# Performance work log

Measured on AMD Instinct MI355X. Metric: run time of the kernel, lower is better.

The kernel has to match this reference:

```python
import jax, jax.numpy as jnp
import numpy as np
from jax import lax

_SOBEL_X = jnp.array([[-1., 0., 1.], [-2., 0., 2.], [-1., 0., 1.]], dtype=jnp.float32)
_SOBEL_Y = jnp.array([[1., 2., 1.], [0., 0., 0.], [-1., -2., -1.]], dtype=jnp.float32)


def rgb2ycrcb(x):
    # x: [B,3,H,W] -> [B,3,H,W] (Y, Cr, Cb)
    R, G, B = x[:, 0], x[:, 1], x[:, 2]
    Y = 0.299 * R + 0.587 * G + 0.114 * B
    Cr = (R - Y) * 0.713 + 0.5
    Cb = (B - Y) * 0.564 + 0.5
    return jnp.stack([Y, Cr, Cb], axis=1)


def depthwise_sobel(x):
    # x: [B,3,H,W]; per-channel 3x3 cross-correlation with SAME padding (matches F.conv2d pad=1)
    C = x.shape[1]
    wx = jnp.broadcast_to(_SOBEL_X[None, None], (C, 1, 3, 3))
    wy = jnp.broadcast_to(_SOBEL_Y[None, None], (C, 1, 3, 3))
    dn = ('NCHW', 'OIHW', 'NCHW')
    gx = lax.conv_general_dilated(x, wx, (1, 1), 'SAME', feature_group_count=C, dimension_numbers=dn)
    gy = lax.conv_general_dilated(x, wy, (1, 1), 'SAME', feature_group_count=C, dimension_numbers=dn)
    return gx, gy


def adjust_gamma(img, gamma, gain=1.0):
    # torchvision float path: clamp(gain * img**gamma, 0, 1)
    return jnp.clip(gain * img ** gamma, 0.0, 1.0)


def adjust_contrast(img, factor):
    # torchvision: blend with per-image mean of grayscale, then clamp
    gray = 0.2989 * img[:, 0:1] + 0.587 * img[:, 1:2] + 0.114 * img[:, 2:3]
    mean = jnp.mean(gray, axis=(1, 2, 3), keepdims=True)
    return jnp.clip(factor * img + (1.0 - factor) * mean, 0.0, 1.0)


def l1(a, b):
    return jnp.mean(jnp.abs(a - b))


def fusion_loss(input_vis, input_ir, output, Mask):
    Fuse = output * Mask
    ycc_fuse = rgb2ycrcb(Fuse)
    Cr_F, Cb_F = ycc_fuse[:, 1:2], ycc_fuse[:, 2:3]

    R_vis = adjust_gamma(input_vis, 0.5, 1.0)
    ycc_vis = rgb2ycrcb(R_vis)
    Cr_V, Cb_V = ycc_vis[:, 1:2], ycc_vis[:, 2:3]

    R_ir = adjust_contrast(input_ir, 1.8)

    fgx, fgy = depthwise_sobel(Fuse)
    vgx, vgy = depthwise_sobel(R_vis)
    igx, igy = depthwise_sobel(R_ir)

    joint_gx = jnp.maximum(vgx, igx)
    joint_gy = jnp.maximum(vgy, igy)
    joint_int = jnp.maximum(R_vis, R_ir)

    con_loss = l1(Fuse, joint_int)
    grad_loss = 0.5 * l1(fgx, joint_gx) + 0.5 * l1(fgy, joint_gy)
    color_loss = l1(Cb_F, Cb_V) + l1(Cr_F, Cr_V)
    return 0.5 * con_loss + 0.2 * grad_loss + 1.0 * color_loss


def setup_inputs() -> dict:
    key = jax.random.key(0)
    k1, k2, k3, k4 = jax.random.split(key, 4)
    B, C, H, W = 16, 3, 512, 512
    return {
        'input_vis': jax.random.uniform(k1, (B, C, H, W), dtype=jnp.float32),
        'input_ir': jax.random.uniform(k2, (B, C, H, W), dtype=jnp.float32),
        'output': jax.random.uniform(k3, (B, C, H, W), dtype=jnp.float32),
        'Mask': jax.random.uniform(k4, (B, C, H, W), dtype=jnp.float32),
    }


def reference(input_vis, input_ir, output, Mask):
    return fusion_loss(input_vis, input_ir, output, Mask)
```

## Files before the change

kernel.cpp:

```cpp
#include <hip/hip_runtime.h>
#include <math.h>

#define Bn 16
#define Cn 3
#define Hn 512
#define Wn 512
#define HWn (Hn*Wn)
#define CHWn (Cn*HWn)
#define Rr 8

__device__ __forceinline__ float clamp01(float x) {
    return fminf(fmaxf(x, 0.0f), 1.0f);
}

__global__ __launch_bounds__(256) void gray_mean_kernel(
        const float* __restrict__ ir, float* __restrict__ ws)
{
    const int b = blockIdx.y;
    const int tid = threadIdx.x;
    const float* base = ir + (size_t)b * CHWn;

    float sr = 0.f, sg = 0.f, sb = 0.f;
#pragma unroll
    for (int k = 0; k < 8; ++k) {
        size_t px = (size_t)blockIdx.x * 8192 + (size_t)(k * 256 + tid) * 4;
        float4 r4 = *(const float4*)(base + px);
        float4 g4 = *(const float4*)(base + HWn + px);
        float4 b4 = *(const float4*)(base + 2 * HWn + px);
        sr += (r4.x + r4.y) + (r4.z + r4.w);
        sg += (g4.x + g4.y) + (g4.z + g4.w);
        sb += (b4.x + b4.y) + (b4.z + b4.w);
    }
    float s = 0.2989f * sr + 0.587f * sg + 0.114f * sb;

#pragma unroll
    for (int off = 32; off; off >>= 1) s += __shfl_down(s, off, 64);

    __shared__ float red[4];
    if ((tid & 63) == 0) red[tid >> 6] = s;
    __syncthreads();
    if (tid == 0) atomicAdd(&ws[b], (red[0] + red[1]) + (red[2] + red[3]));
}

__global__ __launch_bounds__(256) void fusion_main_kernel(
        const float* __restrict__ vis, const float* __restrict__ ir,
        const float* __restrict__ outp, const float* __restrict__ mask,
        float* __restrict__ ws)
{
    const int tid = threadIdx.x;
    const int tx = tid & 127;
    const int sy = tid >> 7;
    const int b  = blockIdx.y;
    const int y0 = (blockIdx.x * 2 + sy) * Rr;
    const int x0 = tx * 4;

    const float mean_b = ws[b] * (1.0f / (float)HWn);
    const float moff = 0.8f * mean_b;

    const size_t bb = (size_t)b * CHWn;
    const float* pv = vis  + bb;
    const float* pi = ir   + bb;
    const float* po = outp + bb;
    const float* pm = mask + bb;

    float conA = 0.f, gxA = 0.f, gyA = 0.f;

    for (int c = 0; c < 3; ++c) {
        const float* v_ = pv + (size_t)c * HWn;
        const float* i_ = pi + (size_t)c * HWn;
        const float* o_ = po + (size_t)c * HWn;
        const float* m_ = pm + (size_t)c * HWn;

        float wf[3][6], wv[3][6], wi[3][6];

        auto load_row = [&](int y, int s) {
            if ((unsigned)y < (unsigned)Hn) {
                size_t o = (size_t)y * Wn + x0;
                float4 o4 = *(const float4*)(o_ + o);
                float4 m4 = *(const float4*)(m_ + o);
                float4 v4 = *(const float4*)(v_ + o);
                float4 i4 = *(const float4*)(i_ + o);
                float oL = 0.f, mL = 0.f, vL = 0.f, iL = 0.f;
                float oR = 0.f, mR = 0.f, vR = 0.f, iR = 0.f;
                if (x0 > 0)      { oL = o_[o - 1]; mL = m_[o - 1]; vL = v_[o - 1]; iL = i_[o - 1]; }
                if (x0 + 4 < Wn) { oR = o_[o + 4]; mR = m_[o + 4]; vR = v_[o + 4]; iR = i_[o + 4]; }

                wf[s][0] = oL * mL;     wf[s][1] = o4.x * m4.x;
                wf[s][2] = o4.y * m4.y; wf[s][3] = o4.z * m4.z;
                wf[s][4] = o4.w * m4.w; wf[s][5] = oR * mR;

                wv[s][0] = clamp01(sqrtf(vL));   wv[s][1] = clamp01(sqrtf(v4.x));
                wv[s][2] = clamp01(sqrtf(v4.y)); wv[s][3] = clamp01(sqrtf(v4.z));
                wv[s][4] = clamp01(sqrtf(v4.w)); wv[s][5] = clamp01(sqrtf(vR));

                wi[s][0] = clamp01(fmaf(1.8f, iL,   -moff));
                wi[s][1] = clamp01(fmaf(1.8f, i4.x, -moff));
                wi[s][2] = clamp01(fmaf(1.8f, i4.y, -moff));
                wi[s][3] = clamp01(fmaf(1.8f, i4.z, -moff));
                wi[s][4] = clamp01(fmaf(1.8f, i4.w, -moff));
                wi[s][5] = clamp01(fmaf(1.8f, iR,   -moff));
                if (x0 == 0)       { wf[s][0] = 0.f; wv[s][0] = 0.f; wi[s][0] = 0.f; }
                if (x0 + 4 >= Wn)  { wf[s][5] = 0.f; wv[s][5] = 0.f; wi[s][5] = 0.f; }
            } else {
#pragma unroll
                for (int k = 0; k < 6; ++k) { wf[s][k] = 0.f; wv[s][k] = 0.f; wi[s][k] = 0.f; }
            }
        };

        load_row(y0 - 1, 0);
        load_row(y0,     1);

        for (int yy = 0; yy < Rr; ++yy) {
            load_row(y0 + yy + 1, 2);

#pragma unroll
            for (int j = 0; j < 4; ++j) {
                float gxf = (wf[0][j+2] - wf[0][j]) + 2.f * (wf[1][j+2] - wf[1][j]) + (wf[2][j+2] - wf[2][j]);
                float gyf = (wf[0][j] + 2.f * wf[0][j+1] + wf[0][j+2]) - (wf[2][j] + 2.f * wf[2][j+1] + wf[2][j+2]);

                float gxv = (wv[0][j+2] - wv[0][j]) + 2.f * (wv[1][j+2] - wv[1][j]) + (wv[2][j+2] - wv[2][j]);
                float gyv = (wv[0][j] + 2.f * wv[0][j+1] + wv[0][j+2]) - (wv[2][j] + 2.f * wv[2][j+1] + wv[2][j+2]);

                float gxi = (wi[0][j+2] - wi[0][j]) + 2.f * (wi[1][j+2] - wi[1][j]) + (wi[2][j+2] - wi[2][j]);
                float gyi = (wi[0][j] + 2.f * wi[0][j+1] + wi[0][j+2]) - (wi[2][j] + 2.f * wi[2][j+1] + wi[2][j+2]);

                gxA  += fabsf(gxf - fmaxf(gxv, gxi));
                gyA  += fabsf(gyf - fmaxf(gyv, gyi));
                conA += fabsf(wf[1][j+1] - fmaxf(wv[1][j+1], wi[1][j+1]));
            }

#pragma unroll
            for (int k = 0; k < 6; ++k) {
                wf[0][k] = wf[1][k]; wf[1][k] = wf[2][k];
                wv[0][k] = wv[1][k]; wv[1][k] = wv[2][k];
                wi[0][k] = wi[1][k]; wi[1][k] = wi[2][k];
            }
        }
    }

    float crA = 0.f, cbA = 0.f;
    {
        auto px = [&](float fr, float fg, float fb, float vr, float vg, float vb) {
            float fY = 0.299f * fr + 0.587f * fg + 0.114f * fb;
            float vY = 0.299f * vr + 0.587f * vg + 0.114f * vb;
            float crf = (fr - fY) * 0.713f, crv = (vr - vY) * 0.713f;
            float cbf = (fb - fY) * 0.564f, cbv = (vb - vY) * 0.564f;
            crA += fabsf(crf - crv);
            cbA += fabsf(cbf - cbv);
        };
        for (int y = y0; y < y0 + Rr; ++y) {
            size_t o = (size_t)y * Wn + x0;
            float4 oR = *(const float4*)(po + o);
            float4 oG = *(const float4*)(po + HWn + o);
            float4 oB = *(const float4*)(po + 2 * HWn + o);
            float4 mR = *(const float4*)(pm + o);
            float4 mG = *(const float4*)(pm + HWn + o);
            float4 mB = *(const float4*)(pm + 2 * HWn + o);
            float4 vR = *(const float4*)(pv + o);
            float4 vG = *(const float4*)(pv + HWn + o);
            float4 vB = *(const float4*)(pv + 2 * HWn + o);
            px(oR.x * mR.x, oG.x * mG.x, oB.x * mB.x,
               clamp01(sqrtf(vR.x)), clamp01(sqrtf(vG.x)), clamp01(sqrtf(vB.x)));
            px(oR.y * mR.y, oG.y * mG.y, oB.y * mB.y,
               clamp01(sqrtf(vR.y)), clamp01(sqrtf(vG.y)), clamp01(sqrtf(vB.y)));
            px(oR.z * mR.z, oG.z * mG.z, oB.z * mB.z,
               clamp01(sqrtf(vR.z)), clamp01(sqrtf(vG.z)), clamp01(sqrtf(vB.z)));
            px(oR.w * mR.w, oG.w * mG.w, oB.w * mB.w,
               clamp01(sqrtf(vR.w)), clamp01(sqrtf(vG.w)), clamp01(sqrtf(vB.w)));
        }
    }

    auto wred = [](float x) {
#pragma unroll
        for (int off = 32; off; off >>= 1) x += __shfl_down(x, off, 64);
        return x;
    };
    conA = wred(conA); gxA = wred(gxA); gyA = wred(gyA);
    crA  = wred(crA);  cbA = wred(cbA);

    __shared__ float red[5][4];
    const int lane = tid & 63, w = tid >> 6;
    if (lane == 0) {
        red[0][w] = conA; red[1][w] = gxA; red[2][w] = gyA;
        red[3][w] = crA;  red[4][w] = cbA;
    }
    __syncthreads();
    if (tid < 5) {
        float s = (red[tid][0] + red[tid][1]) + (red[tid][2] + red[tid][3]);
        atomicAdd(&ws[16 + tid], s);
    }
}

__global__ void finalize_kernel(const float* __restrict__ ws, float* __restrict__ out)
{
    if (threadIdx.x == 0 && blockIdx.x == 0) {
        const float invN3 = 1.0f / (float)((size_t)Bn * Cn * HWn);
        const float invN1 = 1.0f / (float)((size_t)Bn * HWn);
        float con = ws[16] * invN3;
        float gx  = ws[17] * invN3;
        float gy  = ws[18] * invN3;
        float cr  = ws[19] * invN1;
        float cb  = ws[20] * invN1;
        out[0] = 0.5f * con + 0.2f * (0.5f * gx + 0.5f * gy) + (cb + cr);
    }
}

extern "C" void kernel_launch(void* const* d_in, const int* in_sizes, int n_in,
                              void* d_out, int out_size, void* d_ws, size_t ws_size,
                              hipStream_t stream)
{
    const float* vis = (const float*)d_in[0];
    const float* ir  = (const float*)d_in[1];
    const float* out = (const float*)d_in[2];
    const float* msk = (const float*)d_in[3];
    float* ws = (float*)d_ws;

    hipMemsetAsync(ws, 0, 32 * sizeof(float), stream);

    gray_mean_kernel<<<dim3(32, Bn), 256, 0, stream>>>(ir, ws);
    fusion_main_kernel<<<dim3(Hn / (2 * Rr), Bn), 256, 0, stream>>>(vis, ir, out, msk, ws);
    finalize_kernel<<<1, 64, 0, stream>>>(ws, (float*)d_out);
}
```

Baseline: 241.4 us.

## Fuse channels and color loss into single rolling-window pass

```diff
diff --git a/kernel.cpp b/kernel.cpp
--- a/kernel.cpp
+++ b/kernel.cpp
@@ -42,17 +42,15 @@
     if (tid == 0) atomicAdd(&ws[b], (red[0] + red[1]) + (red[2] + red[3]));
 }
 
-__global__ __launch_bounds__(256) void fusion_main_kernel(
+__global__ __launch_bounds__(128, 2) void fusion_main_kernel(
         const float* __restrict__ vis, const float* __restrict__ ir,
         const float* __restrict__ outp, const float* __restrict__ mask,
         float* __restrict__ ws)
 {
     const int tid = threadIdx.x;
-    const int tx = tid & 127;
-    const int sy = tid >> 7;
-    const int b  = blockIdx.y;
-    const int y0 = (blockIdx.x * 2 + sy) * Rr;
-    const int x0 = tx * 4;
+    const int b   = blockIdx.y;
+    const int y0  = blockIdx.x * Rr;
+    const int x0  = tid * 4;
 
     const float mean_b = ws[b] * (1.0f / (float)HWn);
     const float moff = 0.8f * mean_b;
@@ -63,110 +61,90 @@
     const float* po = outp + bb;
     const float* pm = mask + bb;
 
-    float conA = 0.f, gxA = 0.f, gyA = 0.f;
-
-    for (int c = 0; c < 3; ++c) {
-        const float* v_ = pv + (size_t)c * HWn;
-        const float* i_ = pi + (size_t)c * HWn;
-        const float* o_ = po + (size_t)c * HWn;
-        const float* m_ = pm + (size_t)c * HWn;
-
-        float wf[3][6], wv[3][6], wi[3][6];
-
-        auto load_row = [&](int y, int s) {
-            if ((unsigned)y < (unsigned)Hn) {
-                size_t o = (size_t)y * Wn + x0;
-                float4 o4 = *(const float4*)(o_ + o);
-                float4 m4 = *(const float4*)(m_ + o);
-                float4 v4 = *(const float4*)(v_ + o);
-                float4 i4 = *(const float4*)(i_ + o);
+    float wf[3][3][6], wv[3][3][6], wi[3][3][6];
+
+    float conA = 0.f, gxA = 0.f, gyA = 0.f, crA = 0.f, cbA = 0.f;
+
+    auto load_row = [&](int y, int s) {
+        if ((unsigned)y < (unsigned)Hn) {
+            const size_t rowo = (size_t)y * Wn + x0;
+#pragma unroll
+            for (int c = 0; c < 3; ++c) {
+                const float* o_ = po + (size_t)c * HWn;
+                const float* m_ = pm + (size_t)c * HWn;
+                const float* v_ = pv + (size_t)c * HWn;
+                const float* i_ = pi + (size_t)c * HWn;
+                float4 o4 = *(const float4*)(o_ + rowo);
+                float4 m4 = *(const float4*)(m_ + rowo);
+                float4 v4 = *(const float4*)(v_ + rowo);
+                float4 i4 = *(const float4*)(i_ + rowo);
                 float oL = 0.f, mL = 0.f, vL = 0.f, iL = 0.f;
                 float oR = 0.f, mR = 0.f, vR = 0.f, iR = 0.f;
-                if (x0 > 0)      { oL = o_[o - 1]; mL = m_[o - 1]; vL = v_[o - 1]; iL = i_[o - 1]; }
-                if (x0 + 4 < Wn) { oR = o_[o + 4]; mR = m_[o + 4]; vR = v_[o + 4]; iR = i_[o + 4]; }
-
-                wf[s][0] = oL * mL;     wf[s][1] = o4.x * m4.x;
-                wf[s][2] = o4.y * m4.y; wf[s][3] = o4.z * m4.z;
-                wf[s][4] = o4.w * m4.w; wf[s][5] = oR * mR;
-
-                wv[s][0] = clamp01(sqrtf(vL));   wv[s][1] = clamp01(sqrtf(v4.x));
-                wv[s][2] = clamp01(sqrtf(v4.y)); wv[s][3] = clamp01(sqrtf(v4.z));
-                wv[s][4] = clamp01(sqrtf(v4.w)); wv[s][5] = clamp01(sqrtf(vR));
-
-                wi[s][0] = clamp01(fmaf(1.8f, iL,   -moff));
-                wi[s][1] = clamp01(fmaf(1.8f, i4.x, -moff));
-                wi[s][2] = clamp01(fmaf(1.8f, i4.y, -moff));
-                wi[s][3] = clamp01(fmaf(1.8f, i4.z, -moff));
-                wi[s][4] = clamp01(fmaf(1.8f, i4.w, -moff));
-                wi[s][5] = clamp01(fmaf(1.8f, iR,   -moff));
-                if (x0 == 0)       { wf[s][0] = 0.f; wv[s][0] = 0.f; wi[s][0] = 0.f; }
-                if (x0 + 4 >= Wn)  { wf[s][5] = 0.f; wv[s][5] = 0.f; wi[s][5] = 0.f; }
-            } else {
-#pragma unroll
-                for (int k = 0; k < 6; ++k) { wf[s][k] = 0.f; wv[s][k] = 0.f; wi[s][k] = 0.f; }
+                if (x0 > 0)      { oL = o_[rowo - 1]; mL = m_[rowo - 1]; vL = v_[rowo - 1]; iL = i_[rowo - 1]; }
+                if (x0 + 4 < Wn) { oR = o_[rowo + 4]; mR = m_[rowo + 4]; vR = v_[rowo + 4]; iR = i_[rowo + 4]; }
+
+                wf[c][s][0] = oL * mL;     wf[c][s][1] = o4.x * m4.x;
+                wf[c][s][2] = o4.y * m4.y; wf[c][s][3] = o4.z * m4.z;
+                wf[c][s][4] = o4.w * m4.w; wf[c][s][5] = oR * mR;
+
+                wv[c][s][0] = clamp01(sqrtf(vL));   wv[c][s][1] = clamp01(sqrtf(v4.x));
+                wv[c][s][2] = clamp01(sqrtf(v4.y)); wv[c][s][3] = clamp01(sqrtf(v4.z));
+                wv[c][s][4] = clamp01(sqrtf(v4.w)); wv[c][s][5] = clamp01(sqrtf(vR));
+
+                wi[c][s][0] = clamp01(fmaf(1.8f, iL,   -moff));
+                wi[c][s][1] = clamp01(fmaf(1.8f, i4.x, -moff));
+                wi[c][s][2] = clamp01(fmaf(1.8f, i4.y, -moff));
+                wi[c][s][3] = clamp01(fmaf(1.8f, i4.z, -moff));
+                wi[c][s][4] = clamp01(fmaf(1.8f, i4.w, -moff));
+                wi[c][s][5] = clamp01(fmaf(1.8f, iR,   -moff));
             }
-        };
-
-        load_row(y0 - 1, 0);
-        load_row(y0,     1);
-
-        for (int yy = 0; yy < Rr; ++yy) {
-            load_row(y0 + yy + 1, 2);
-
-#pragma unroll
-            for (int j = 0; j < 4; ++j) {
-                float gxf = (wf[0][j+2] - wf[0][j]) + 2.f * (wf[1][j+2] - wf[1][j]) + (wf[2][j+2] - wf[2][j]);
-                float gyf = (wf[0][j] + 2.f * wf[0][j+1] + wf[0][j+2]) - (wf[2][j] + 2.f * wf[2][j+1] + wf[2][j+2]);
-
-                float gxv = (wv[0][j+2] - wv[0][j]) + 2.f * (wv[1][j+2] - wv[1][j]) + (wv[2][j+2] - wv[2][j]);
-                float gyv = (wv[0][j] + 2.f * wv[0][j+1] + wv[0][j+2]) - (wv[2][j] + 2.f * wv[2][j+1] + wv[2][j+2]);
-
-                float gxi = (wi[0][j+2] - wi[0][j]) + 2.f * (wi[1][j+2] - wi[1][j]) + (wi[2][j+2] - wi[2][j]);
-                float gyi = (wi[0][j] + 2.f * wi[0][j+1] + wi[0][j+2]) - (wi[2][j] + 2.f * wi[2][j+1] + wi[2][j+2]);
-
-                gxA  += fabsf(gxf - fmaxf(gxv, gxi));
-                gyA  += fabsf(gyf - fmaxf(gyv, gyi));
-                conA += fabsf(wf[1][j+1] - fmaxf(wv[1][j+1], wi[1][j+1]));
+        } else {
+#pragma unroll
+            for (int c = 0; c < 3; ++c)
+#pragma unroll
+                for (int k = 0; k < 6; ++k) {
+                    wf[c][s][k] = 0.f; wv[c][s][k] = 0.f; wi[c][s][k] = 0.f;
+                }
+        }
+    };
+
+    load_row(y0 - 1, 0);
+    load_row(y0,     1);
+
+#pragma unroll
+    for (int yy = 0; yy < Rr; ++yy) {
+        const int sA = (yy    ) % 3;
+        const int sB = (yy + 1) % 3;
+        const int sC = (yy + 2) % 3;
+        load_row(y0 + yy + 1, sC);
+
+#pragma unroll
+        for (int j = 0; j < 4; ++j) {
+            float cf[3], cv[3];
+#pragma unroll
+            for (int c = 0; c < 3; ++c) {
+                float gxf = (wf[c][sA][j+2] - wf[c][sA][j]) + 2.f * (wf[c][sB][j+2] - wf[c][sB][j]) + (wf[c][sC][j+2] - wf[c][sC][j]);
+                float gyf = (wf[c][sA][j] + 2.f * wf[c][sA][j+1] + wf[c][sA][j+2]) - (wf[c][sC][j] + 2.f * wf[c][sC][j+1] + wf[c][sC][j+2]);
+
+                float gxv = (wv[c][sA][j+2] - wv[c][sA][j]) + 2.f * (wv[c][sB][j+2] - wv[c][sB][j]) + (wv[c][sC][j+2] - wv[c][sC][j]);
+                float gyv = (wv[c][sA][j] + 2.f * wv[c][sA][j+1] + wv[c][sA][j+2]) - (wv[c][sC][j] + 2.f * wv[c][sC][j+1] + wv[c][sC][j+2]);
+
+                float gxi = (wi[c][sA][j+2] - wi[c][sA][j]) + 2.f * (wi[c][sB][j+2] - wi[c][sB][j]) + (wi[c][sC][j+2] - wi[c][sC][j]);
+                float gyi = (wi[c][sA][j] + 2.f * wi[c][sA][j+1] + wi[c][sA][j+2]) - (wi[c][sC][j] + 2.f * wi[c][sC][j+1] + wi[c][sC][j+2]);
+
+                gxA += fabsf(gxf - fmaxf(gxv, gxi));
+                gyA += fabsf(gyf - fmaxf(gyv, gyi));
+
+                float f1 = wf[c][sB][j+1];
+                float v1 = wv[c][sB][j+1];
+                float i1 = wi[c][sB][j+1];
+                conA += fabsf(f1 - fmaxf(v1, i1));
+                cf[c] = f1; cv[c] = v1;
             }
-
-#pragma unroll
-            for (int k = 0; k < 6; ++k) {
-                wf[0][k] = wf[1][k]; wf[1][k] = wf[2][k];
-                wv[0][k] = wv[1][k]; wv[1][k] = wv[2][k];
-                wi[0][k] = wi[1][k]; wi[1][k] = wi[2][k];
-            }
-        }
-    }
-
-    float crA = 0.f, cbA = 0.f;
-    {
-        auto px = [&](float fr, float fg, float fb, float vr, float vg, float vb) {
-            float fY = 0.299f * fr + 0.587f * fg + 0.114f * fb;
-            float vY = 0.299f * vr + 0.587f * vg + 0.114f * vb;
-            float crf = (fr - fY) * 0.713f, crv = (vr - vY) * 0.713f;
-            float cbf = (fb - fY) * 0.564f, cbv = (vb - vY) * 0.564f;
-            crA += fabsf(crf - crv);
-            cbA += fabsf(cbf - cbv);
-        };
-        for (int y = y0; y < y0 + Rr; ++y) {
-            size_t o = (size_t)y * Wn + x0;
-            float4 oR = *(const float4*)(po + o);
-            float4 oG = *(const float4*)(po + HWn + o);
-            float4 oB = *(const float4*)(po + 2 * HWn + o);
-            float4 mR = *(const float4*)(pm + o);
-            float4 mG = *(const float4*)(pm + HWn + o);
-            float4 mB = *(const float4*)(pm + 2 * HWn + o);
-            float4 vR = *(const float4*)(pv + o);
-            float4 vG = *(const float4*)(pv + HWn + o);
-            float4 vB = *(const float4*)(pv + 2 * HWn + o);
-            px(oR.x * mR.x, oG.x * mG.x, oB.x * mB.x,
-               clamp01(sqrtf(vR.x)), clamp01(sqrtf(vG.x)), clamp01(sqrtf(vB.x)));
-            px(oR.y * mR.y, oG.y * mG.y, oB.y * mB.y,
-               clamp01(sqrtf(vR.y)), clamp01(sqrtf(vG.y)), clamp01(sqrtf(vB.y)));
-            px(oR.z * mR.z, oG.z * mG.z, oB.z * mB.z,
-               clamp01(sqrtf(vR.z)), clamp01(sqrtf(vG.z)), clamp01(sqrtf(vB.z)));
-            px(oR.w * mR.w, oG.w * mG.w, oB.w * mB.w,
-               clamp01(sqrtf(vR.w)), clamp01(sqrtf(vG.w)), clamp01(sqrtf(vB.w)));
+            float fY = 0.299f * cf[0] + 0.587f * cf[1] + 0.114f * cf[2];
+            float vY = 0.299f * cv[0] + 0.587f * cv[1] + 0.114f * cv[2];
+            crA += fabsf((cf[0] - fY) * 0.713f - (cv[0] - vY) * 0.713f);
+            cbA += fabsf((cf[2] - fY) * 0.564f - (cv[2] - vY) * 0.564f);
         }
     }
 
@@ -178,7 +156,7 @@
     conA = wred(conA); gxA = wred(gxA); gyA = wred(gyA);
     crA  = wred(crA);  cbA = wred(cbA);
 
-    __shared__ float red[5][4];
+    __shared__ float red[5][2];
     const int lane = tid & 63, w = tid >> 6;
     if (lane == 0) {
         red[0][w] = conA; red[1][w] = gxA; red[2][w] = gyA;
@@ -186,8 +164,7 @@
     }
     __syncthreads();
     if (tid < 5) {
-        float s = (red[tid][0] + red[tid][1]) + (red[tid][2] + red[tid][3]);
-        atomicAdd(&ws[16 + tid], s);
+        atomicAdd(&ws[16 + tid], red[tid][0] + red[tid][1]);
     }
 }
 
@@ -218,6 +195,6 @@
     hipMemsetAsync(ws, 0, 32 * sizeof(float), stream);
 
     gray_mean_kernel<<<dim3(32, Bn), 256, 0, stream>>>(ir, ws);
-    fusion_main_kernel<<<dim3(Hn / (2 * Rr), Bn), 256, 0, stream>>>(vis, ir, out, msk, ws);
+    fusion_main_kernel<<<dim3(Hn / Rr, Bn), 128, 0, stream>>>(vis, ir, out, msk, ws);
     finalize_kernel<<<1, 64, 0, stream>>>(ws, (float*)d_out);
 }
```

Measured after the change: 335.3 us. 1.39x slower.
